# Performance work log

Measured on AMD Instinct MI355X. Metric: run time of the kernel, lower is better.

## Reference

```python
import jax, jax.numpy as jnp
import numpy as np

HEAD_SIZE = 64
EMBED = 512


def setup_inputs() -> dict:
    key = jax.random.key(0)
    kx, kk, kq, kv = jax.random.split(key, 4)
    x = jax.random.normal(kx, (4, 4096, EMBED), dtype=jnp.float32)
    # torch Linear(EMBED, HEAD_SIZE, bias=False) weight: [HEAD_SIZE, EMBED]
    scale = 1.0 / np.sqrt(EMBED)
    Wk = jax.random.normal(kk, (HEAD_SIZE, EMBED), dtype=jnp.float32) * scale
    Wq = jax.random.normal(kq, (HEAD_SIZE, EMBED), dtype=jnp.float32) * scale
    Wv = jax.random.normal(kv, (HEAD_SIZE, EMBED), dtype=jnp.float32) * scale
    return {"x": x, "Wk": Wk, "Wq": Wq, "Wv": Wv}


def reference(x, Wk, Wq, Wv):
    B, T, C = x.shape
    # projections: x @ W.T  -> [B, T, H]
    k = jnp.einsum('btc,hc->bth', x, Wk)
    q = jnp.einsum('btc,hc->bth', x, Wq)
    v = jnp.einsum('btc,hc->bth', x, Wv)
    # scores scaled by C**-0.5 (input embed dim, as in the source module)
    scores = jnp.einsum('bth,bsh->bts', q, k) * (C ** -0.5)  # [B, T, T]
    causal = jnp.tril(jnp.ones((T, T), dtype=bool))
    scores = jnp.where(causal, scores, -jnp.inf)
    weights = jax.nn.softmax(scores, axis=-1)
    # dropout p=0.0 -> identity
    out = jnp.einsum('bts,bsh->bth', weights, v)  # [B, T, H]
    return out
```

## Files before the change

kernel.cpp:

```cpp
#include <hip/hip_runtime.h>

typedef unsigned short u16;
typedef unsigned int   u32;

#define NB 4
#define NT 4096
#define NC 512
#define NH 64
#define ATT_SCALE 0.044194173824159216f
#define LOG2E     1.4426950408889634f
#define QSCALE    (ATT_SCALE * LOG2E)
#define NEG_BIG   -30000.0f
#define ITEMS_PB  1088
#define ITEMS2_PB 2176

typedef __attribute__((ext_vector_type(8))) _Float16 half8;
typedef __attribute__((ext_vector_type(4))) _Float16 half4;
typedef __attribute__((ext_vector_type(4))) float    floatx4;


__global__ __launch_bounds__(256) void wconv(
    const float* __restrict__ Wk, const float* __restrict__ Wq,
    const float* __restrict__ Wv, _Float16* __restrict__ Wh)
{
    const int gid = blockIdx.x * 256 + threadIdx.x;
    const int w = gid >> 13;
    const int i = gid & 8191;
    const int h = i >> 7, c = (i & 127) * 4;
    const float* src = (w == 0) ? Wq : (w == 1) ? Wk : Wv;
    const float sc = (w == 0) ? QSCALE : 1.0f;
    float4 f = *(const float4*)&src[h * NC + c];
    half4 o = {(_Float16)(f.x * sc), (_Float16)(f.y * sc),
               (_Float16)(f.z * sc), (_Float16)(f.w * sc)};
    const int blk = ((w * 16 + (c >> 5)) * 4 + (h >> 4));
    *(half4*)&Wh[(size_t)blk * 512 + (h & 15) * 32 + ((c >> 3) & 3) * 8 + (c & 7)] = o;
}

__global__ __launch_bounds__(256) void qkv_mfma(
    const float* __restrict__ x, const _Float16* __restrict__ Wh,
    _Float16* __restrict__ Qf, _Float16* __restrict__ Kf,
    _Float16* __restrict__ Vf)
{
    __shared__ __align__(16) floatx4 red[3][12][64];

    const int tid  = threadIdx.x;
    const int wv   = tid >> 6;
    const int lane = tid & 63;
    const int quad = lane >> 4;
    const int id   = lane & 15;
    const int rowbase = blockIdx.x * 16;

    floatx4 acc[3][4] = {};
    const float* xp = x + (size_t)(rowbase + id) * NC + wv * 128;
    const int loff = id * 32 + quad * 8;

#pragma unroll
    for (int ks = 0; ks < 4; ++ks) {
        float4 f0 = *(const float4*)&xp[ks * 32 + quad * 8];
        float4 f1 = *(const float4*)&xp[ks * 32 + quad * 8 + 4];
        half8 a;
        a[0] = (_Float16)f0.x; a[1] = (_Float16)f0.y;
        a[2] = (_Float16)f0.z; a[3] = (_Float16)f0.w;
        a[4] = (_Float16)f1.x; a[5] = (_Float16)f1.y;
        a[6] = (_Float16)f1.z; a[7] = (_Float16)f1.w;
        const int ksg = wv * 4 + ks;
#pragma unroll
        for (int w = 0; w < 3; ++w)
#pragma unroll
            for (int nt = 0; nt < 4; ++nt) {
                half8 bf = *(const half8*)&Wh[(size_t)((w * 16 + ksg) * 4 + nt) * 512 + loff];
                acc[w][nt] = __builtin_amdgcn_mfma_f32_16x16x32_f16(a, bf, acc[w][nt], 0, 0, 0);
            }
    }

    if (wv) {
#pragma unroll
        for (int w = 0; w < 3; ++w)
#pragma unroll
            for (int nt = 0; nt < 4; ++nt)
                red[wv - 1][w * 4 + nt][lane] = acc[w][nt];
    }
    __syncthreads();
    if (wv) return;

#pragma unroll
    for (int w = 0; w < 3; ++w)
#pragma unroll
        for (int nt = 0; nt < 4; ++nt) {
            floatx4 a0 = red[0][w * 4 + nt][lane];
            floatx4 a1 = red[1][w * 4 + nt][lane];
            floatx4 a2 = red[2][w * 4 + nt][lane];
            acc[w][nt] += a0 + a1 + a2;
        }

    const int b  = rowbase >> 12, L = rowbase & 4095;
    const int q16 = L >> 4, kt = L >> 6, tt = (L >> 4) & 3;
    const int kop = ((rowbase & 63) + quad * 4) >> 5;
    const int q4k = ((((rowbase & 63) + quad * 4) >> 3) & 3);
#pragma unroll
    for (int nt = 0; nt < 4; ++nt) {
        const int hop = nt >> 1;
        const int q4h = (nt * 2 + (id >> 3)) & 3;
        const int j   = id & 7;
        const size_t qa = (size_t)((b * 256 + q16) * 2 + hop) * 512 + q4h * 8 + j;
        const size_t ka = (size_t)(((b * 64 + kt) * 4 + tt) * 2 + hop) * 512 + q4h * 8 + j;
#pragma unroll
        for (int r = 0; r < 4; ++r) {
            Qf[qa + (quad * 4 + r) * 32] = (_Float16)acc[0][nt][r];
            Kf[ka + (quad * 4 + r) * 32] = (_Float16)acc[1][nt][r];
        }
        half4 vh = {(_Float16)acc[2][nt][0], (_Float16)acc[2][nt][1],
                    (_Float16)acc[2][nt][2], (_Float16)acc[2][nt][3]};
        const size_t va = (size_t)(((b * 64 + kt) * 4 + nt) * 2 + kop) * 512
                        + id * 32 + q4k * 8 + (quad & 1) * 4;
        *(half4*)&Vf[va] = vh;
    }
}

__global__ __launch_bounds__(256, 6) void attn_part(
    const _Float16* __restrict__ Qf, const _Float16* __restrict__ Kf,
    const _Float16* __restrict__ Vf, _Float16* __restrict__ Opart,
    float2* __restrict__ MLpart)
{
    constexpr int KP = 72;
    __shared__ __align__(16) _Float16 Ps[4][16 * KP];

    const int tid  = threadIdx.x;
    const int wv   = tid >> 6;
    const int lane = tid & 63;
    const int quad = lane >> 4;
    const int id   = lane & 15;
    const int item2 = blockIdx.x * 4 + wv;
    const int item  = item2 >> 1;
    const int st    = item2 & 1;
    const int b     = blockIdx.y;
    const int loff  = id * 32 + quad * 8;

    int m = (int)((1.0f + __builtin_sqrtf((float)item + 1.0f)) * 0.5f);
    while (4 * m * (m + 1) <= item) ++m;
    while (m > 1 && 4 * m * (m - 1) > item) --m;
    const int rem  = item - 4 * m * (m - 1);
    const int qs   = 8 * (m - 1) + rem / m;
    const int seg  = rem - (rem / m) * m;
    const int ntiles = (qs >> 1) + 1;
    const int t0 = seg * ntiles / m;
    const int t1 = (seg + 1) * ntiles / m;

    const size_t qa = (size_t)((b * 256 + qs * 2 + st) * 2) * 512 + loff;
    half8 qb0 = *(const half8*)&Qf[qa];
    half8 qb1 = *(const half8*)&Qf[qa + 512];

    floatx4 o[4] = {};
    float m_i = NEG_BIG, l_i = 0.f;

    for (int kt = t0; kt < t1; ++kt) {
        const size_t tb = (size_t)((b * 64 + kt) * 4) * 2 * 512;

        floatx4 s4[4] = {};
#pragma unroll
        for (int t = 0; t < 4; ++t) {
            half8 ka0 = *(const half8*)&Kf[tb + (size_t)t * 1024 + loff];
            half8 ka1 = *(const half8*)&Kf[tb + (size_t)t * 1024 + 512 + loff];
            s4[t] = __builtin_amdgcn_mfma_f32_16x16x32_f16(ka0, qb0, s4[t], 0, 0, 0);
            s4[t] = __builtin_amdgcn_mfma_f32_16x16x32_f16(ka1, qb1, s4[t], 0, 0, 0);
        }

        half8 va00 = *(const half8*)&Vf[tb + loff];
        half8 va01 = *(const half8*)&Vf[tb + 512 + loff];

        if (kt == ntiles - 1) {
            const int kb = kt * 64;
            const int qrow = qs * 32 + st * 16 + id;
#pragma unroll
            for (int t = 0; t < 4; ++t)
#pragma unroll
                for (int r = 0; r < 4; ++r)
                    if (kb + 16 * t + quad * 4 + r > qrow)
                        s4[t][r] = NEG_BIG;
        }

        float mx = s4[0][0];
#pragma unroll
        for (int t = 0; t < 4; ++t)
#pragma unroll
            for (int r = 0; r < 4; ++r) mx = fmaxf(mx, s4[t][r]);
        mx = fmaxf(mx, __shfl_xor(mx, 16));
        mx = fmaxf(mx, __shfl_xor(mx, 32));
        const float mnew  = fmaxf(m_i, mx);
        const float alpha = exp2f(m_i - mnew);
        m_i = mnew;
        float psum = 0.f;
#pragma unroll
        for (int t = 0; t < 4; ++t)
#pragma unroll
            for (int r = 0; r < 4; ++r) {
                float p = exp2f(s4[t][r] - mnew);
                s4[t][r] = p;
                psum += p;
            }
        psum += __shfl_xor(psum, 16);
        psum += __shfl_xor(psum, 32);
        l_i = l_i * alpha + psum;

#pragma unroll
        for (int t = 0; t < 4; ++t) {
            half4 ph = {(_Float16)s4[t][0], (_Float16)s4[t][1],
                        (_Float16)s4[t][2], (_Float16)s4[t][3]};
            *(half4*)&Ps[wv][id * KP + 16 * t + quad * 4] = ph;
        }
#pragma unroll
        for (int t = 0; t < 4; ++t)
#pragma unroll
            for (int r = 0; r < 4; ++r) o[t][r] *= alpha;

        half8 pb0 = *(const half8*)&Ps[wv][id * KP + quad * 8];
        half8 pb1 = *(const half8*)&Ps[wv][id * KP + 32 + quad * 8];

        o[0] = __builtin_amdgcn_mfma_f32_16x16x32_f16(va00, pb0, o[0], 0, 0, 0);
        o[0] = __builtin_amdgcn_mfma_f32_16x16x32_f16(va01, pb1, o[0], 0, 0, 0);
#pragma unroll
        for (int t = 1; t < 4; ++t) {
            half8 v0 = *(const half8*)&Vf[tb + (size_t)t * 1024 + loff];
            half8 v1 = *(const half8*)&Vf[tb + (size_t)t * 1024 + 512 + loff];
            o[t] = __builtin_amdgcn_mfma_f32_16x16x32_f16(v0, pb0, o[t], 0, 0, 0);
            o[t] = __builtin_amdgcn_mfma_f32_16x16x32_f16(v1, pb1, o[t], 0, 0, 0);
        }
    }

    const int p = b * ITEMS2_PB + item2;
    const float rl = 1.f / l_i;
#pragma unroll
    for (int t = 0; t < 4; ++t) {
        half4 oh = {(_Float16)(o[t][0] * rl), (_Float16)(o[t][1] * rl),
                    (_Float16)(o[t][2] * rl), (_Float16)(o[t][3] * rl)};
        *(half4*)&Ps[wv][id * KP + 16 * t + quad * 4] = oh;
    }
    const int rr = lane >> 3, rc = (lane & 7) * 8;
    half8 u0 = *(const half8*)&Ps[wv][rr * KP + rc];
    half8 u1 = *(const half8*)&Ps[wv][(8 + rr) * KP + rc];
    _Float16* ob = &Opart[(size_t)(p * 16) * NH];
    *(half8*)&ob[rr * NH + rc] = u0;
    *(half8*)&ob[(8 + rr) * NH + rc] = u1;

    if (quad == 0)
        MLpart[p * 16 + id] = make_float2(m_i, l_i);
}

__global__ __launch_bounds__(256) void attn_combine(
    const _Float16* __restrict__ Opart, const float2* __restrict__ MLpart,
    float* __restrict__ out)
{
    const int qs = blockIdx.x, b = blockIdx.y;
    const int tid = threadIdx.x;
    const int row = tid >> 3;
    const int hc  = tid & 7;
    const int lid = tid & 63;
    const int sst = row >> 4, r16 = row & 15;
    const int m = (qs >> 3) + 1;
    const int base0 = 4 * m * (m - 1) + (qs - 8 * (m - 1)) * m;

    auto gidx = [&](int k) -> size_t {
        return (size_t)(b * ITEMS2_PB + (base0 + k) * 2 + sst) * 16 + r16;
    };

    float2 ml0 = make_float2(NEG_BIG, 0.f), ml1 = make_float2(NEG_BIG, 0.f);
    if (hc < m)     ml0 = MLpart[gidx(hc)];
    if (hc + 8 < m) ml1 = MLpart[gidx(hc + 8)];
    float M = fmaxf(ml0.x, ml1.x);
    M = fmaxf(M, __shfl_xor(M, 1));
    M = fmaxf(M, __shfl_xor(M, 2));
    M = fmaxf(M, __shfl_xor(M, 4));
    const float w0 = ml0.y * exp2f(ml0.x - M);
    const float w1 = ml1.y * exp2f(ml1.x - M);
    float W = w0 + w1;
    W += __shfl_xor(W, 1);
    W += __shfl_xor(W, 2);
    W += __shfl_xor(W, 4);

    float acc[8] = {};
    for (int k0 = 0; k0 < m; k0 += 4) {
        const int c0 = k0,     c1 = (k0 + 1 < m) ? k0 + 1 : m - 1;
        const int c2 = (k0 + 2 < m) ? k0 + 2 : m - 1;
        const int c3 = (k0 + 3 < m) ? k0 + 3 : m - 1;
        half8 o0 = *(const half8*)&Opart[gidx(c0) * NH + hc * 8];
        half8 o1 = *(const half8*)&Opart[gidx(c1) * NH + hc * 8];
        half8 o2 = *(const half8*)&Opart[gidx(c2) * NH + hc * 8];
        half8 o3 = *(const half8*)&Opart[gidx(c3) * NH + hc * 8];
#pragma unroll
        for (int i = 0; i < 4; ++i) {
            const int k = k0 + i;
            const float wsrc = (k < 8) ? w0 : w1;
            float ws = __shfl(wsrc, (lid & 56) | (k & 7));
            if (k >= m) ws = 0.f;
            const half8 oh = (i == 0) ? o0 : (i == 1) ? o1 : (i == 2) ? o2 : o3;
#pragma unroll
            for (int j = 0; j < 8; ++j) acc[j] += ws * (float)oh[j];
        }
    }
    const float rl = 1.f / W;
    float* dst = out + (size_t)(b * NT + qs * 32 + row) * NH + hc * 8;
#pragma unroll
    for (int j = 0; j < 8; ++j) dst[j] = acc[j] * rl;
}

extern "C" void kernel_launch(void* const* d_in, const int* in_sizes, int n_in,
                              void* d_out, int out_size, void* d_ws, size_t ws_size,
                              hipStream_t stream) {
    const float* x  = (const float*)d_in[0];
    const float* Wk = (const float*)d_in[1];
    const float* Wq = (const float*)d_in[2];
    const float* Wv = (const float*)d_in[3];

    char* wsb = (char*)d_ws;
    _Float16* Qf    = (_Float16*)wsb;
    _Float16* Kf    = Qf + 1048576;
    _Float16* Vf    = Kf + 1048576;
    _Float16* Wh    = Vf + 1048576;
    float2*   MLpart= (float2*)(wsb + 6488064);
    _Float16* Opart = (_Float16*)(wsb + 7602176);

    wconv<<<96, 256, 0, stream>>>(Wk, Wq, Wv, Wh);
    qkv_mfma<<<1024, 256, 0, stream>>>(x, Wh, Qf, Kf, Vf);
    attn_part<<<dim3(ITEMS2_PB / 4, NB), 256, 0, stream>>>(Qf, Kf, Vf, Opart, MLpart);
    attn_combine<<<dim3(128, NB), 256, 0, stream>>>(Opart, MLpart, (float*)d_out);
}
```

Before: 144.7 us.

## Prefetch K/V tiles, lazy softmax rescale, split QKV epilogue, unroll combine

```diff
diff --git a/kernel.cpp b/kernel.cpp
--- a/kernel.cpp
+++ b/kernel.cpp
@@ -54,10 +54,15 @@
     const float* xp = x + (size_t)(rowbase + id) * NC + wv * 128;
     const int loff = id * 32 + quad * 8;
 
+    float4 xr[8];
+#pragma unroll
+    for (int ksq = 0; ksq < 8; ++ksq)
+        xr[ksq] = *(const float4*)&xp[(ksq >> 1) * 32 + quad * 8 + (ksq & 1) * 4];
+
 #pragma unroll
     for (int ks = 0; ks < 4; ++ks) {
-        float4 f0 = *(const float4*)&xp[ks * 32 + quad * 8];
-        float4 f1 = *(const float4*)&xp[ks * 32 + quad * 8 + 4];
+        float4 f0 = xr[2 * ks];
+        float4 f1 = xr[2 * ks + 1];
         half8 a;
         a[0] = (_Float16)f0.x; a[1] = (_Float16)f0.y;
         a[2] = (_Float16)f0.z; a[3] = (_Float16)f0.w;
@@ -73,51 +78,51 @@
             }
     }
 
-    if (wv) {
-#pragma unroll
-        for (int w = 0; w < 3; ++w)
-#pragma unroll
-            for (int nt = 0; nt < 4; ++nt)
-                red[wv - 1][w * 4 + nt][lane] = acc[w][nt];
+#pragma unroll
+    for (int idx = 0; idx < 12; ++idx) {
+        const int ow = idx / 3;
+        if (ow != wv)
+            red[(wv > ow) ? wv - 1 : wv][idx][lane] = acc[idx >> 2][idx & 3];
     }
     __syncthreads();
-    if (wv) return;
-
-#pragma unroll
-    for (int w = 0; w < 3; ++w)
-#pragma unroll
-        for (int nt = 0; nt < 4; ++nt) {
-            floatx4 a0 = red[0][w * 4 + nt][lane];
-            floatx4 a1 = red[1][w * 4 + nt][lane];
-            floatx4 a2 = red[2][w * 4 + nt][lane];
-            acc[w][nt] += a0 + a1 + a2;
-        }
 
     const int b  = rowbase >> 12, L = rowbase & 4095;
     const int q16 = L >> 4, kt = L >> 6, tt = (L >> 4) & 3;
     const int kop = ((rowbase & 63) + quad * 4) >> 5;
     const int q4k = ((((rowbase & 63) + quad * 4) >> 3) & 3);
-#pragma unroll
-    for (int nt = 0; nt < 4; ++nt) {
-        const int hop = nt >> 1;
-        const int q4h = (nt * 2 + (id >> 3)) & 3;
-        const int j   = id & 7;
-        const size_t qa = (size_t)((b * 256 + q16) * 2 + hop) * 512 + q4h * 8 + j;
-        const size_t ka = (size_t)(((b * 64 + kt) * 4 + tt) * 2 + hop) * 512 + q4h * 8 + j;
-#pragma unroll
-        for (int r = 0; r < 4; ++r) {
-            Qf[qa + (quad * 4 + r) * 32] = (_Float16)acc[0][nt][r];
-            Kf[ka + (quad * 4 + r) * 32] = (_Float16)acc[1][nt][r];
-        }
-        half4 vh = {(_Float16)acc[2][nt][0], (_Float16)acc[2][nt][1],
-                    (_Float16)acc[2][nt][2], (_Float16)acc[2][nt][3]};
-        const size_t va = (size_t)(((b * 64 + kt) * 4 + nt) * 2 + kop) * 512
-                        + id * 32 + q4k * 8 + (quad & 1) * 4;
-        *(half4*)&Vf[va] = vh;
-    }
-}
-
-__global__ __launch_bounds__(256, 6) void attn_part(
+
+#define QKV_EPIL(IDX) do {                                                     \
+    constexpr int w_ = (IDX) >> 2, nt_ = (IDX) & 3;                            \
+    floatx4 a_ = acc[w_][nt_];                                                 \
+    a_ += red[0][IDX][lane] + red[1][IDX][lane] + red[2][IDX][lane];           \
+    if (w_ == 0 || w_ == 1) {                                                  \
+        const int hop = nt_ >> 1;                                              \
+        const int q4h = (nt_ * 2 + (id >> 3)) & 3;                             \
+        const int j   = id & 7;                                                \
+        const size_t ad = (w_ == 0)                                            \
+            ? (size_t)((b * 256 + q16) * 2 + hop) * 512 + q4h * 8 + j          \
+            : (size_t)(((b * 64 + kt) * 4 + tt) * 2 + hop) * 512 + q4h * 8 + j;\
+        _Float16* dstp = (w_ == 0) ? Qf : Kf;                                  \
+        _Pragma("unroll")                                                      \
+        for (int r = 0; r < 4; ++r)                                            \
+            dstp[ad + (quad * 4 + r) * 32] = (_Float16)a_[r];                  \
+    } else {                                                                   \
+        half4 vh = {(_Float16)a_[0], (_Float16)a_[1],                          \
+                    (_Float16)a_[2], (_Float16)a_[3]};                         \
+        const size_t va = (size_t)(((b * 64 + kt) * 4 + nt_) * 2 + kop) * 512  \
+                        + id * 32 + q4k * 8 + (quad & 1) * 4;                  \
+        *(half4*)&Vf[va] = vh;                                                 \
+    }                                                                          \
+} while (0)
+
+    if (wv == 0)      { QKV_EPIL(0); QKV_EPIL(1);  QKV_EPIL(2);  }
+    else if (wv == 1) { QKV_EPIL(3); QKV_EPIL(4);  QKV_EPIL(5);  }
+    else if (wv == 2) { QKV_EPIL(6); QKV_EPIL(7);  QKV_EPIL(8);  }
+    else              { QKV_EPIL(9); QKV_EPIL(10); QKV_EPIL(11); }
+#undef QKV_EPIL
+}
+
+__global__ __launch_bounds__(256, 4) void attn_part(
     const _Float16* __restrict__ Qf, const _Float16* __restrict__ Kf,
     const _Float16* __restrict__ Vf, _Float16* __restrict__ Opart,
     float2* __restrict__ MLpart)
@@ -147,26 +152,34 @@
     const int t1 = (seg + 1) * ntiles / m;
 
     const size_t qa = (size_t)((b * 256 + qs * 2 + st) * 2) * 512 + loff;
-    half8 qb0 = *(const half8*)&Qf[qa];
-    half8 qb1 = *(const half8*)&Qf[qa + 512];
+    const half8 qb0 = *(const half8*)&Qf[qa];
+    const half8 qb1 = *(const half8*)&Qf[qa + 512];
 
     floatx4 o[4] = {};
-    float m_i = NEG_BIG, l_i = 0.f;
+    float m_i = NEG_BIG;
+    float l_q = 0.f;
+
+    size_t tb = (size_t)((b * 64 + t0) * 8) * 512 + loff;
+    half8 kc[8], kn[8], vc[8];
+#pragma unroll
+    for (int t = 0; t < 8; ++t) kc[t] = *(const half8*)&Kf[tb + (size_t)t * 512];
 
     for (int kt = t0; kt < t1; ++kt) {
-        const size_t tb = (size_t)((b * 64 + kt) * 4) * 2 * 512;
+#pragma unroll
+        for (int t = 0; t < 8; ++t) vc[t] = *(const half8*)&Vf[tb + (size_t)t * 512];
+        const bool more = (kt + 1 < t1);
+        if (more) {
+#pragma unroll
+            for (int t = 0; t < 8; ++t)
+                kn[t] = *(const half8*)&Kf[tb + 4096 + (size_t)t * 512];
+        }
 
         floatx4 s4[4] = {};
 #pragma unroll
         for (int t = 0; t < 4; ++t) {
-            half8 ka0 = *(const half8*)&Kf[tb + (size_t)t * 1024 + loff];
-            half8 ka1 = *(const half8*)&Kf[tb + (size_t)t * 1024 + 512 + loff];
-            s4[t] = __builtin_amdgcn_mfma_f32_16x16x32_f16(ka0, qb0, s4[t], 0, 0, 0);
-            s4[t] = __builtin_amdgcn_mfma_f32_16x16x32_f16(ka1, qb1, s4[t], 0, 0, 0);
-        }
-
-        half8 va00 = *(const half8*)&Vf[tb + loff];
-        half8 va01 = *(const half8*)&Vf[tb + 512 + loff];
+            s4[t] = __builtin_amdgcn_mfma_f32_16x16x32_f16(kc[2 * t],     qb0, s4[t], 0, 0, 0);
+            s4[t] = __builtin_amdgcn_mfma_f32_16x16x32_f16(kc[2 * t + 1], qb1, s4[t], 0, 0, 0);
+        }
 
         if (kt == ntiles - 1) {
             const int kb = kt * 64;
@@ -179,28 +192,36 @@
                         s4[t][r] = NEG_BIG;
         }
 
-        float mx = s4[0][0];
+        float pmax = s4[0][0];
 #pragma unroll
         for (int t = 0; t < 4; ++t)
 #pragma unroll
-            for (int r = 0; r < 4; ++r) mx = fmaxf(mx, s4[t][r]);
-        mx = fmaxf(mx, __shfl_xor(mx, 16));
-        mx = fmaxf(mx, __shfl_xor(mx, 32));
-        const float mnew  = fmaxf(m_i, mx);
-        const float alpha = exp2f(m_i - mnew);
-        m_i = mnew;
+            for (int r = 0; r < 4; ++r) pmax = fmaxf(pmax, s4[t][r]);
+
+        if (__any(pmax > m_i + 8.0f)) {
+            float mx = pmax;
+            mx = fmaxf(mx, __shfl_xor(mx, 16));
+            mx = fmaxf(mx, __shfl_xor(mx, 32));
+            const float mnew  = fmaxf(m_i, mx);
+            const float alpha = exp2f(m_i - mnew);
+            m_i = mnew;
+            l_q *= alpha;
+#pragma unroll
+            for (int t = 0; t < 4; ++t)
+#pragma unroll
+                for (int r = 0; r < 4; ++r) o[t][r] *= alpha;
+        }
+
         float psum = 0.f;
 #pragma unroll
         for (int t = 0; t < 4; ++t)
 #pragma unroll
             for (int r = 0; r < 4; ++r) {
-                float p = exp2f(s4[t][r] - mnew);
+                const float p = exp2f(s4[t][r] - m_i);
                 s4[t][r] = p;
                 psum += p;
             }
-        psum += __shfl_xor(psum, 16);
-        psum += __shfl_xor(psum, 32);
-        l_i = l_i * alpha + psum;
+        l_q += psum;
 
 #pragma unroll
         for (int t = 0; t < 4; ++t) {
@@ -208,27 +229,28 @@
                         (_Float16)s4[t][2], (_Float16)s4[t][3]};
             *(half4*)&Ps[wv][id * KP + 16 * t + quad * 4] = ph;
         }
-#pragma unroll
-        for (int t = 0; t < 4; ++t)
-#pragma unroll
-            for (int r = 0; r < 4; ++r) o[t][r] *= alpha;
-
-        half8 pb0 = *(const half8*)&Ps[wv][id * KP + quad * 8];
-        half8 pb1 = *(const half8*)&Ps[wv][id * KP + 32 + quad * 8];
-
-        o[0] = __builtin_amdgcn_mfma_f32_16x16x32_f16(va00, pb0, o[0], 0, 0, 0);
-        o[0] = __builtin_amdgcn_mfma_f32_16x16x32_f16(va01, pb1, o[0], 0, 0, 0);
-#pragma unroll
-        for (int t = 1; t < 4; ++t) {
-            half8 v0 = *(const half8*)&Vf[tb + (size_t)t * 1024 + loff];
-            half8 v1 = *(const half8*)&Vf[tb + (size_t)t * 1024 + 512 + loff];
-            o[t] = __builtin_amdgcn_mfma_f32_16x16x32_f16(v0, pb0, o[t], 0, 0, 0);
-            o[t] = __builtin_amdgcn_mfma_f32_16x16x32_f16(v1, pb1, o[t], 0, 0, 0);
-        }
-    }
+        const half8 pb0 = *(const half8*)&Ps[wv][id * KP + quad * 8];
+        const half8 pb1 = *(const half8*)&Ps[wv][id * KP + 32 + quad * 8];
+
+#pragma unroll
+        for (int t = 0; t < 4; ++t) {
+            o[t] = __builtin_amdgcn_mfma_f32_16x16x32_f16(vc[2 * t],     pb0, o[t], 0, 0, 0);
+            o[t] = __builtin_amdgcn_mfma_f32_16x16x32_f16(vc[2 * t + 1], pb1, o[t], 0, 0, 0);
+        }
+
+        if (more) {
+#pragma unroll
+            for (int t = 0; t < 8; ++t) kc[t] = kn[t];
+        }
+        tb += 4096;
+    }
+
+    float l_t = l_q;
+    l_t += __shfl_xor(l_t, 16);
+    l_t += __shfl_xor(l_t, 32);
 
     const int p = b * ITEMS2_PB + item2;
-    const float rl = 1.f / l_i;
+    const float rl = 1.f / l_t;
 #pragma unroll
     for (int t = 0; t < 4; ++t) {
         half4 oh = {(_Float16)(o[t][0] * rl), (_Float16)(o[t][1] * rl),
@@ -243,7 +265,7 @@
     *(half8*)&ob[(8 + rr) * NH + rc] = u1;
 
     if (quad == 0)
-        MLpart[p * 16 + id] = make_float2(m_i, l_i);
+        MLpart[p * 16 + id] = make_float2(m_i, l_t);
 }
 
 __global__ __launch_bounds__(256) void attn_combine(
@@ -254,7 +276,6 @@
     const int tid = threadIdx.x;
     const int row = tid >> 3;
     const int hc  = tid & 7;
-    const int lid = tid & 63;
     const int sst = row >> 4, r16 = row & 15;
     const int m = (qs >> 3) + 1;
     const int base0 = 4 * m * (m - 1) + (qs - 8 * (m - 1)) * m;
@@ -263,40 +284,31 @@
         return (size_t)(b * ITEMS2_PB + (base0 + k) * 2 + sst) * 16 + r16;
     };
 
-    float2 ml0 = make_float2(NEG_BIG, 0.f), ml1 = make_float2(NEG_BIG, 0.f);
-    if (hc < m)     ml0 = MLpart[gidx(hc)];
-    if (hc + 8 < m) ml1 = MLpart[gidx(hc + 8)];
-    float M = fmaxf(ml0.x, ml1.x);
-    M = fmaxf(M, __shfl_xor(M, 1));
-    M = fmaxf(M, __shfl_xor(M, 2));
-    M = fmaxf(M, __shfl_xor(M, 4));
-    const float w0 = ml0.y * exp2f(ml0.x - M);
-    const float w1 = ml1.y * exp2f(ml1.x - M);
-    float W = w0 + w1;
-    W += __shfl_xor(W, 1);
-    W += __shfl_xor(W, 2);
-    W += __shfl_xor(W, 4);
+    float2 ml[16];
+#pragma unroll
+    for (int k = 0; k < 16; ++k)
+        ml[k] = MLpart[gidx(k < m ? k : 0)];
+
+    float M = NEG_BIG;
+#pragma unroll
+    for (int k = 0; k < 16; ++k)
+        if (k < m) M = fmaxf(M, ml[k].x);
+
+    float w[16], W = 0.f;
+#pragma unroll
+    for (int k = 0; k < 16; ++k) {
+        const float wk = (k < m) ? ml[k].y * exp2f(ml[k].x - M) : 0.f;
+        w[k] = wk; W += wk;
+    }
 
     float acc[8] = {};
-    for (int k0 = 0; k0 < m; k0 += 4) {
-        const int c0 = k0,     c1 = (k0 + 1 < m) ? k0 + 1 : m - 1;
-        const int c2 = (k0 + 2 < m) ? k0 + 2 : m - 1;
-        const int c3 = (k0 + 3 < m) ? k0 + 3 : m - 1;
-        half8 o0 = *(const half8*)&Opart[gidx(c0) * NH + hc * 8];
-        half8 o1 = *(const half8*)&Opart[gidx(c1) * NH + hc * 8];
-        half8 o2 = *(const half8*)&Opart[gidx(c2) * NH + hc * 8];
-        half8 o3 = *(const half8*)&Opart[gidx(c3) * NH + hc * 8];
-#pragma unroll
-        for (int i = 0; i < 4; ++i) {
-            const int k = k0 + i;
-            const float wsrc = (k < 8) ? w0 : w1;
-            float ws = __shfl(wsrc, (lid & 56) | (k & 7));
-            if (k >= m) ws = 0.f;
-            const half8 oh = (i == 0) ? o0 : (i == 1) ? o1 : (i == 2) ? o2 : o3;
-#pragma unroll
-            for (int j = 0; j < 8; ++j) acc[j] += ws * (float)oh[j];
-        }
-    }
+#pragma unroll
+    for (int k = 0; k < 16; ++k) {
+        const half8 oh = *(const half8*)&Opart[gidx(k < m ? k : 0) * NH + hc * 8];
+#pragma unroll
+        for (int j = 0; j < 8; ++j) acc[j] += w[k] * (float)oh[j];
+    }
+
     const float rl = 1.f / W;
     float* dst = out + (size_t)(b * NT + qs * 32 + row) * NH + hc * 8;
 #pragma unroll
```

Result: slower. 149.8 us (+3.5%).
